# Kernel optimization log

Measured on AMD Instinct MI355X. Metric: run time of the kernel, lower is better.

Reference implementation:

```python
import jax, jax.numpy as jnp
import numpy as np


def setup_inputs() -> dict:
    key = jax.random.key(0)
    k1, k2 = jax.random.split(key)
    inputs = jax.random.normal(k1, (4, 128, 64, 64), dtype=jnp.float32)
    # binary hole mask (1 = known background, 0 = hole), broadcast over channels
    mask = jnp.round(jax.random.uniform(k2, (4, 1, 64, 64), dtype=jnp.float32))
    return {"inputs": inputs, "mask": mask}


def reference(inputs, mask):
    # SFFA contextual attention with 1x1 dynamic kernels.
    # Note: in the original torch code the 1x1 conv with padding=1 produces
    # border scores that conv_transpose2d with padding=1 crops away exactly,
    # so the math reduces to per-pixel matmul + softmax + matmul.
    bz, nc, h, w = inputs.shape
    N = h * w
    background = inputs * mask                              # [b, c, h, w]
    # dynamic kernels: one nc-dim vector per background pixel (patch)
    K = background.reshape(bz, nc, N).transpose(0, 2, 1) + 1e-7   # [b, N, c]
    Kn = K / jnp.sqrt(jnp.sum(K * K, axis=2, keepdims=True))      # l2-normalized
    feat = inputs.reshape(bz, nc, N)                        # [b, c, N]
    scores = jnp.einsum('bpc,bcn->bpn', Kn, feat)           # [b, N(patch), N(pixel)]
    attn = jax.nn.softmax(scores, axis=1)                   # softmax over patches p
    agg = jnp.einsum('bpc,bpn->bcn', K, attn).reshape(bz, nc, h, w)
    return background + agg * (1.0 - mask)
```

## Files before the change

### kernel.cpp

```cpp
#include <hip/hip_runtime.h>
#include <hip/hip_bf16.h>

typedef __attribute__((ext_vector_type(8))) short bf16x8;
typedef __attribute__((ext_vector_type(4))) float f32x4;

#define NPIX 4096
#define NC   128
#define RS128 0.08838834764831845f

#define GL2LDS(g, l) __builtin_amdgcn_global_load_lds( \
    (const __attribute__((address_space(1))) void*)(g), \
    (__attribute__((address_space(3))) void*)(l), 16, 0, 0)

__global__ __launch_bounds__(1024) void sffa_prep(
    const float* __restrict__ x, const float* __restrict__ mask,
    ushort* __restrict__ KnW, ushort* __restrict__ QW, ushort* __restrict__ VtW,
    float* __restrict__ s0c, int* __restrict__ pixQ, int* __restrict__ cnts,
    float* __restrict__ out)
{
    __shared__ float xs[128][69];
    __shared__ float ms[64];
    __shared__ float rinv[64];
    __shared__ float ssum[64];
    __shared__ float2 part[16][64];
    __shared__ int se[64];
    __shared__ int bgn[64];
    __shared__ int tinfo[2];
    __shared__ int wredP[16], wredT[16];
    const int tid = threadIdx.x;
    const int b = blockIdx.x >> 6, nblk = blockIdx.x & 63;
    const int n0 = nblk * 64;
    const float* xb = x + (size_t)b * NC * NPIX;
    float* ob = out + (size_t)b * NC * NPIX;

    #pragma unroll
    for (int it = 0; it < 2; ++it) {
        int e4 = it * 1024 + tid;
        int c = e4 >> 4, n4 = (e4 & 15) * 4;
        float4 v = *(const float4*)(xb + (size_t)c * NPIX + n0 + n4);
        xs[c][n4+0] = v.x; xs[c][n4+1] = v.y; xs[c][n4+2] = v.z; xs[c][n4+3] = v.w;
        *(float4*)(ob + (size_t)c * NPIX + n0 + n4) = v;
    }
    if (tid < 16) {
        float4 mv = *(const float4*)(mask + (size_t)b * NPIX + n0 + tid * 4);
        ms[tid*4+0] = mv.x; ms[tid*4+1] = mv.y; ms[tid*4+2] = mv.z; ms[tid*4+3] = mv.w;
    }
    {
        const int lane = tid & 63, w = tid >> 6;
        float4 mv = *(const float4*)(mask + (size_t)b * NPIX + tid * 4);
        int f0 = mv.x < 0.5f ? 0x10000 : 1;
        int f1 = mv.y < 0.5f ? 0x10000 : 1;
        int f2 = mv.z < 0.5f ? 0x10000 : 1;
        int f3 = mv.w < 0.5f ? 0x10000 : 1;
        int p0 = tid * 4;
        int pre = 0, tot = f0 + f1 + f2 + f3;
        if (p0 + 0 < n0) pre += f0;
        if (p0 + 1 < n0) pre += f1;
        if (p0 + 2 < n0) pre += f2;
        if (p0 + 3 < n0) pre += f3;
        #pragma unroll
        for (int d = 1; d < 64; d <<= 1) {
            pre += __shfl_xor(pre, d);
            tot += __shfl_xor(tot, d);
        }
        if (lane == 0) { wredP[w] = pre; wredT[w] = tot; }
    }
    __syncthreads();
    if (tid < 64) {
        int vP = (tid < 16) ? wredP[tid] : 0;
        int vT = (tid < 16) ? wredT[tid] : 0;
        #pragma unroll
        for (int d = 1; d < 16; d <<= 1) {
            vP += __shfl_xor(vP, d);
            vT += __shfl_xor(vT, d);
        }
        int base  = __shfl(vP, 0);
        int total = __shfl(vT, 0);
        if (tid == 0 && nblk == 0) {
            cnts[b * 2]     = total & 0xffff;
            cnts[b * 2 + 1] = total >> 16;
        }
        int f = ms[tid] > 0.5f ? 1 : 0x10000;
        int s = f;
        #pragma unroll
        for (int d = 1; d < 64; d <<= 1) {
            int t = __shfl_up(s, d);
            if (tid >= d) s += t;
        }
        se[tid] = base + s - f;
    }
    __syncthreads();
    {
        int p = tid & 63, qd = tid >> 6;
        float m = ms[p];
        float s2 = 0.f, s1 = 0.f;
        #pragma unroll
        for (int i = 0; i < 8; ++i) {
            float xv = xs[qd*8 + i][p];
            float k = fmaf(xv, m, 1e-7f);
            s2 = fmaf(k, k, s2);
            s1 += xv;
        }
        part[qd][p] = make_float2(s2, s1);
    }
    __syncthreads();
    if (tid < 64) {
        float s2 = 0.f, s1 = 0.f;
        #pragma unroll
        for (int k = 0; k < 16; ++k) { float2 t = part[k][tid]; s2 += t.x; s1 += t.y; }
        rinv[tid] = rsqrtf(s2);
        ssum[tid] = s1 * RS128;
    }
    __syncthreads();
    #pragma unroll
    for (int it = 0; it < 4; ++it) {
        int e2 = it * 1024 + tid;
        int n = e2 >> 6, cp = (e2 & 63) * 2;
        int pe = se[n];
        float x0 = xs[cp][n], x1 = xs[cp+1][n];
        if (ms[n] > 0.5f) {
            int slot = pe & 0xffff;
            float k0 = x0 + 1e-7f, k1 = x1 + 1e-7f;
            float r = rinv[n];
            __hip_bfloat162 kn;
            kn.x = __float2bfloat16(k0 * r); kn.y = __float2bfloat16(k1 * r);
            *(__hip_bfloat162*)(KnW + ((size_t)b * NPIX + slot) * NC + cp) = kn;
        } else {
            int slot = pe >> 16;
            __hip_bfloat162 q;
            q.x = __float2bfloat16(x0); q.y = __float2bfloat16(x1);
            *(__hip_bfloat162*)(QW + ((size_t)b * NPIX + slot) * NC + cp) = q;
        }
    }
    if (tid < 64) {
        if (ms[tid] < 0.5f) {
            int slot = se[tid] >> 16;
            s0c [(size_t)b * NPIX + slot] = ssum[tid];
            pixQ[(size_t)b * NPIX + slot] = n0 + tid;
        } else {
            bgn[(se[tid] & 0xffff) - (se[0] & 0xffff)] = tid;
        }
    }
    if (tid == 0) {
        tinfo[0] = se[0] & 0xffff;
        tinfo[1] = (se[63] & 0xffff) + (ms[63] > 0.5f ? 1 : 0) - (se[0] & 0xffff);
    }
    __syncthreads();
    {
        const int s0b = tinfo[0], nbg = tinfo[1];
        const int j = tid & 63, cg = tid >> 6;
        if (j < nbg) {
            int n = bgn[j];
            ushort* vcol = VtW + (size_t)b * NC * NPIX + s0b + j;
            #pragma unroll
            for (int cc = 0; cc < 8; ++cc) {
                int c = cg * 8 + cc;
                __hip_bfloat16 h = __float2bfloat16(xs[c][n] + 1e-7f);
                vcol[(size_t)c * NPIX] = *(ushort*)&h;
            }
        }
    }
}

#define L_BUF 32768
#define L_P   65536
#define L_ML  75776
#define L_SZ  76800

__global__ __launch_bounds__(512, 4) void sffa_attn(
    const ushort* __restrict__ KnW, const ushort* __restrict__ QW,
    const ushort* __restrict__ VtW, const int* __restrict__ cnts,
    ushort* __restrict__ partW, float* __restrict__ mlW, int KS)
{
    __shared__ __align__(16) char smem[L_SZ];
    const int tid  = threadIdx.x;
    const int w = tid >> 6, lane = tid & 63;
    const int l15 = lane & 15, g = lane >> 4;
    const int bx = (int)blockIdx.x;
    const int per = 64 * KS;
    const int b = bx / per;
    const int rem = bx - b * per;
    const int qblk = rem / KS, ks = rem - (rem / KS) * KS;
    const int q0 = qblk * 64;
    const int cntK = cnts[b * 2], cntQ = cnts[b * 2 + 1];
    if (q0 >= cntQ) return;
    const int blk = (b * 64 + qblk) * KS + ks;

    const int nk64 = (cntK + 63) >> 6;
    const int tpk  = (nk64 + KS - 1) / KS;
    const int t0   = ks * tpk;
    const int NTK  = min(t0 + tpk, nk64) - t0;

    if (NTK <= 0) {
        unsigned* pz = (unsigned*)(partW + (size_t)blk * 8192);
        #pragma unroll
        for (int i = 0; i < 8; ++i) pz[i * 512 + tid] = 0u;
        if (tid < 64)
            *(float2*)(mlW + ((size_t)blk * 64 + tid) * 2) = make_float2(-1e30f, 0.f);
        return;
    }

    const int half = w >> 2;
    const int wq   = w & 3;
    const int kbase = t0 * 64;

    const ushort* Knb = KnW + (size_t)b * NPIX * NC;
    const ushort* Vtb = VtW + (size_t)b * NC * NPIX;

    bf16x8 qf[4];
    {
        const ushort* Qrow = QW + ((size_t)b * NPIX + q0 + wq * 16 + l15) * NC;
        #pragma unroll
        for (int kc = 0; kc < 4; ++kc)
            qf[kc] = *(const bf16x8*)(Qrow + 32 * kc + 8 * g);
    }

    const int rK = tid >> 4;
    const char* srcK = (const char*)(Knb + (size_t)(kbase + rK) * NC)
                     + (((tid & 15) ^ (rK & 15)) << 4);
    const int rV = tid >> 3;
    const char* srcV = (const char*)(Vtb + (size_t)rV * NPIX + kbase)
                     + (((tid & 7) ^ (rV & 7)) << 4);
    char* d0 = smem + tid * 16;

    GL2LDS(srcK,        d0);
    GL2LDS(srcK + 8192, d0 + 8192);
    GL2LDS(srcV,                           d0 + 16384);
    GL2LDS(srcV + (size_t)64 * NPIX * 2,   d0 + 24576);
    __syncthreads();

    f32x4 acc[8];
    const f32x4 fzero = {0.f, 0.f, 0.f, 0.f};
    #pragma unroll
    for (int i = 0; i < 8; ++i) acc[i] = fzero;
    float mrun = -1e30f, lrun = 0.f;
    char* Pw = smem + L_P + w * 1280;

    for (int kt = 0; kt < NTK; ++kt) {
        if (kt + 1 < NTK) {
            char* nb = smem + ((kt + 1) & 1) * L_BUF + tid * 16;
            const char* sK = srcK + (size_t)(kt + 1) * 16384;
            const char* sV = srcV + (size_t)(kt + 1) * 128;
            GL2LDS(sK,        nb);
            GL2LDS(sK + 8192, nb + 8192);
            GL2LDS(sV,                         nb + 16384);
            GL2LDS(sV + (size_t)64 * NPIX * 2, nb + 24576);
        }
        char* bb = smem + (kt & 1) * L_BUF;
        f32x4 sa0 = fzero, sa1 = fzero;
        {
            const char* rb0 = bb + (half * 32 + l15) * 256;
            const char* rb1 = rb0 + 4096;
            const int sw = l15 << 4;
            __builtin_amdgcn_s_setprio(1);
            #pragma unroll
            for (int kc = 0; kc < 4; ++kc) {
                int off = (64 * kc + 16 * g) ^ sw;
                bf16x8 a0 = *(const bf16x8*)(rb0 + off);
                bf16x8 a1 = *(const bf16x8*)(rb1 + off);
                sa0 = __builtin_amdgcn_mfma_f32_16x16x32_bf16(a0, qf[kc], sa0, 0, 0, 0);
                sa1 = __builtin_amdgcn_mfma_f32_16x16x32_bf16(a1, qf[kc], sa1, 0, 0, 0);
            }
            __builtin_amdgcn_s_setprio(0);
        }
        {
            int kg0 = (t0 + kt) * 64;
            if (kg0 + 64 > cntK) {
                int kb = cntK - kg0;
                int kr = half * 32 + 4 * g;
                #pragma unroll
                for (int r = 0; r < 4; ++r) {
                    if (kr + r >= kb)      sa0[r] = -3e38f;
                    if (kr + 16 + r >= kb) sa1[r] = -3e38f;
                }
            }
        }
        float tmax = fmaxf(fmaxf(fmaxf(sa0[0], sa0[1]), fmaxf(sa0[2], sa0[3])),
                           fmaxf(fmaxf(sa1[0], sa1[1]), fmaxf(sa1[2], sa1[3])));
        tmax = fmaxf(tmax, __shfl_xor(tmax, 16));
        tmax = fmaxf(tmax, __shfl_xor(tmax, 32));
        bool grow = !__all(tmax <= mrun + 8.f);
        float mnew = grow ? fmaxf(mrun, tmax) : mrun;
        float p0[4], p1[4];
        float ts = 0.f;
        #pragma unroll
        for (int r = 0; r < 4; ++r) { p0[r] = __expf(sa0[r] - mnew); ts += p0[r]; }
        #pragma unroll
        for (int r = 0; r < 4; ++r) { p1[r] = __expf(sa1[r] - mnew); ts += p1[r]; }
        ts += __shfl_xor(ts, 16);
        ts += __shfl_xor(ts, 32);
        if (grow) {
            float sc = __expf(mrun - mnew);
            lrun = lrun * sc + ts;
            float scr[4];
            #pragma unroll
            for (int r = 0; r < 4; ++r) scr[r] = __shfl(sc, 4 * g + r);
            #pragma unroll
            for (int ct = 0; ct < 8; ++ct) {
                acc[ct][0] *= scr[0]; acc[ct][1] *= scr[1];
                acc[ct][2] *= scr[2]; acc[ct][3] *= scr[3];
            }
            mrun = mnew;
        } else {
            lrun += ts;
        }
        union { __hip_bfloat162 h; unsigned u; } ua0, ua1, ub0, ub1;
        ua0.h.x = __float2bfloat16(p0[0]); ua0.h.y = __float2bfloat16(p0[1]);
        ua1.h.x = __float2bfloat16(p0[2]); ua1.h.y = __float2bfloat16(p0[3]);
        ub0.h.x = __float2bfloat16(p1[0]); ub0.h.y = __float2bfloat16(p1[1]);
        ub1.h.x = __float2bfloat16(p1[2]); ub1.h.y = __float2bfloat16(p1[3]);
        *(int2*)(Pw + l15 * 80 +      8 * g) = make_int2((int)ua0.u, (int)ua1.u);
        *(int2*)(Pw + l15 * 80 + 32 + 8 * g) = make_int2((int)ub0.u, (int)ub1.u);
        bf16x8 pf = *(const bf16x8*)(Pw + l15 * 80 + 16 * g);
        {
            const char* vb = bb + 16384;
            __builtin_amdgcn_s_setprio(1);
            #pragma unroll
            for (int ct = 0; ct < 8; ++ct) {
                int c = 16 * ct + l15;
                bf16x8 vf = *(const bf16x8*)(vb + c * 128 +
                                             ((64 * half + 16 * g) ^ ((c & 7) << 4)));
                acc[ct] = __builtin_amdgcn_mfma_f32_16x16x32_bf16(pf, vf, acc[ct], 0, 0, 0);
            }
            __builtin_amdgcn_s_setprio(0);
        }
        __syncthreads();
    }

    float* ma = (float*)(smem + L_ML);
    float* la = ma + 64; float* mb = la + 64; float* lb = mb + 64;
    const int q = wq * 16 + l15;
    if (g == 0) {
        if (half == 0) { ma[q] = mrun; la[q] = lrun; }
        else           { mb[q] = mrun; lb[q] = lrun; }
    }
    __syncthreads();
    float* agg = (float*)smem;
    {
        float mstar = fmaxf(ma[q], mb[q]);
        float f = __expf(mrun - mstar);
        float fr[4];
        #pragma unroll
        for (int r = 0; r < 4; ++r) fr[r] = __shfl(f, 4 * g + r);
        if (half == 1) {
            #pragma unroll
            for (int ct = 0; ct < 8; ++ct) {
                int c = 16 * ct + l15;
                #pragma unroll
                for (int r = 0; r < 4; ++r)
                    agg[c * 68 + wq * 16 + 4 * g + r] = acc[ct][r] * fr[r];
            }
        }
        __syncthreads();
        if (half == 0) {
            #pragma unroll
            for (int ct = 0; ct < 8; ++ct) {
                int c = 16 * ct + l15;
                #pragma unroll
                for (int r = 0; r < 4; ++r) {
                    int idx = c * 68 + wq * 16 + 4 * g + r;
                    agg[idx] = acc[ct][r] * fr[r] + agg[idx];
                }
            }
        }
    }
    __syncthreads();
    if (tid < 64) {
        float M = fmaxf(ma[tid], mb[tid]);
        float ls = la[tid] * __expf(ma[tid] - M) + lb[tid] * __expf(mb[tid] - M);
        *(float2*)(mlW + ((size_t)blk * 64 + tid) * 2) = make_float2(M, ls);
    }
    ushort* pdst = partW + (size_t)blk * 8192;
    #pragma unroll
    for (int it = 0; it < 8; ++it) {
        int idx = it * 512 + tid;
        int c = idx >> 5, n2 = (idx & 31) * 2;
        __hip_bfloat162 h;
        h.x = __float2bfloat16(agg[c * 68 + n2]);
        h.y = __float2bfloat16(agg[c * 68 + n2 + 1]);
        *(__hip_bfloat162*)(pdst + c * 64 + n2) = h;
    }
}

__global__ __launch_bounds__(256) void sffa_comb(
    const ushort* __restrict__ partW, const float* __restrict__ mlW,
    const float* __restrict__ s0c, const int* __restrict__ pixQ,
    const int* __restrict__ cnts, float* __restrict__ out, int KS)
{
    __shared__ float wgtL[4][64];
    __shared__ int pixnL[64];
    const int tid = threadIdx.x;
    const int bx = blockIdx.x;
    const int b = bx >> 7, qb = (bx >> 1) & 63, ch = bx & 1;
    const int cntK = cnts[b * 2], cntQ = cnts[b * 2 + 1];
    if (qb * 64 >= cntQ) return;
    const int blkbase = (b * 64 + qb) * KS;
    const float m0f = (float)(NPIX - cntK);

    if (tid < 64) {
        int slot = qb * 64 + tid;
        int pix = -1;
        if (slot < cntQ) {
            pix = pixQ[(size_t)b * NPIX + slot];
            float s0 = s0c[(size_t)b * NPIX + slot];
            float M = s0;
            float2 mls[4];
            #pragma unroll
            for (int k = 0; k < 4; ++k) {
                if (k < KS) {
                    mls[k] = *(const float2*)(mlW + ((size_t)(blkbase + k) * 64 + tid) * 2);
                    M = fmaxf(M, mls[k].x);
                }
            }
            float L = m0f * __expf(s0 - M);
            #pragma unroll
            for (int k = 0; k < 4; ++k)
                if (k < KS) L += mls[k].y * __expf(mls[k].x - M);
            float Li = 1.f / L;
            #pragma unroll
            for (int k = 0; k < 4; ++k)
                if (k < KS) wgtL[k][tid] = __expf(mls[k].x - M) * Li;
        }
        pixnL[tid] = pix;
    }
    __syncthreads();

    float* ob = out + ((size_t)b * NC + ch * 64) * NPIX;
    const ushort* pb = partW + (size_t)blkbase * 8192 + ch * 4096;
    #pragma unroll
    for (int it = 0; it < 2; ++it) {
        int idx = it * 256 + tid;
        int c = idx >> 3, grp = idx & 7;
        float v[8] = {0.f,0.f,0.f,0.f,0.f,0.f,0.f,0.f};
        #pragma unroll
        for (int k = 0; k < 4; ++k) {
            if (k < KS) {
                ushort u[8];
                *(int4*)u = *(const int4*)(pb + (size_t)k * 8192 + c * 64 + grp * 8);
                #pragma unroll
                for (int j = 0; j < 8; ++j)
                    v[j] = fmaf(__uint_as_float((unsigned)u[j] << 16),
                                wgtL[k][grp * 8 + j], v[j]);
            }
        }
        #pragma unroll
        for (int j = 0; j < 8; ++j) {
            int pix = pixnL[grp * 8 + j];
            if (pix >= 0) ob[(size_t)c * NPIX + pix] = v[j];
        }
    }
}

extern "C" void kernel_launch(void* const* d_in, const int* in_sizes, int n_in,
                              void* d_out, int out_size, void* d_ws, size_t ws_size,
                              hipStream_t stream) {
    const float* x    = (const float*)d_in[0];
    const float* mask = (const float*)d_in[1];
    char* ws = (char*)d_ws;
    const size_t MBy = 1024 * 1024;
    const size_t KBy = 1024;

    ushort* KnW = (ushort*)(ws);
    ushort* QW  = (ushort*)(ws + 4 * MBy);
    ushort* VtW = (ushort*)(ws + 8 * MBy);

    size_t need4 = 12 * MBy + 16 * MBy + 1 * MBy;
    int KS = (ws_size >= need4) ? 4 : 2;
    ushort* partW = (ushort*)(ws + 12 * MBy);
    char* tail = ws + 12 * MBy + (size_t)KS * 4 * MBy;
    float* mlW  = (float*)(tail);
    float* s0c  = (float*)(tail + 576 * KBy);
    int*   pixQ = (int*)(tail + 640 * KBy);
    int*   cnts = (int*)(tail + 704 * KBy);

    sffa_prep <<<256, 1024, 0, stream>>>(x, mask, KnW, QW, VtW, s0c, pixQ, cnts,
                                         (float*)d_out);
    sffa_attn <<<4 * 64 * KS, 512, 0, stream>>>(KnW, QW, VtW, cnts, partW, mlW, KS);
    sffa_comb <<<4 * 128, 256, 0, stream>>>(partW, mlW, s0c, pixQ, cnts,
                                            (float*)d_out, KS);
}
```

Baseline: 54.56 us.

## Single-buffer attention LDS and raise key split to six for occupancy

The attention kernel drops its double-buffered K/V LDS staging in favour of one buffer that is refilled after each tile's compute under a barrier. This shrinks shared memory per block from about 75KB to about 43KB, so the launch bound can rise to 6 blocks per CU. The key split is fixed at 6 instead of a runtime 2 or 4, giving more parallel blocks, with the combine kernel and workspace layout adjusted to match. In exchange, global-to-LDS loads no longer overlap compute within a block, and the workspace-size fallback is removed, which assumes the larger partial buffer always fits.

Result: slower. 64.39 us (+18.0%).

```diff
diff --git a/kernel.cpp b/kernel.cpp
--- a/kernel.cpp
+++ b/kernel.cpp
@@ -7,6 +7,7 @@
 #define NPIX 4096
 #define NC   128
 #define RS128 0.08838834764831845f
+#define KSP  6
 
 #define GL2LDS(g, l) __builtin_amdgcn_global_load_lds( \
     (const __attribute__((address_space(1))) void*)(g), \
@@ -162,32 +163,32 @@
     }
 }
 
-#define L_BUF 32768
-#define L_P   65536
-#define L_ML  75776
-#define L_SZ  76800
-
-__global__ __launch_bounds__(512, 4) void sffa_attn(
+#define L_V   16384
+#define L_P   32768
+#define L_ML  43008
+#define L_SZ  44032
+
+__global__ __launch_bounds__(512, 6) void sffa_attn(
     const ushort* __restrict__ KnW, const ushort* __restrict__ QW,
     const ushort* __restrict__ VtW, const int* __restrict__ cnts,
-    ushort* __restrict__ partW, float* __restrict__ mlW, int KS)
+    ushort* __restrict__ partW, float* __restrict__ mlW)
 {
     __shared__ __align__(16) char smem[L_SZ];
     const int tid  = threadIdx.x;
     const int w = tid >> 6, lane = tid & 63;
     const int l15 = lane & 15, g = lane >> 4;
     const int bx = (int)blockIdx.x;
-    const int per = 64 * KS;
+    const int per = 64 * KSP;
     const int b = bx / per;
     const int rem = bx - b * per;
-    const int qblk = rem / KS, ks = rem - (rem / KS) * KS;
+    const int qblk = rem / KSP, ks = rem - (rem / KSP) * KSP;
     const int q0 = qblk * 64;
     const int cntK = cnts[b * 2], cntQ = cnts[b * 2 + 1];
     if (q0 >= cntQ) return;
-    const int blk = (b * 64 + qblk) * KS + ks;
+    const int blk = (b * 64 + qblk) * KSP + ks;
 
     const int nk64 = (cntK + 63) >> 6;
-    const int tpk  = (nk64 + KS - 1) / KS;
+    const int tpk  = (nk64 + KSP - 1) / KSP;
     const int t0   = ks * tpk;
     const int NTK  = min(t0 + tpk, nk64) - t0;
 
@@ -237,19 +238,9 @@
     char* Pw = smem + L_P + w * 1280;
 
     for (int kt = 0; kt < NTK; ++kt) {
-        if (kt + 1 < NTK) {
-            char* nb = smem + ((kt + 1) & 1) * L_BUF + tid * 16;
-            const char* sK = srcK + (size_t)(kt + 1) * 16384;
-            const char* sV = srcV + (size_t)(kt + 1) * 128;
-            GL2LDS(sK,        nb);
-            GL2LDS(sK + 8192, nb + 8192);
-            GL2LDS(sV,                         nb + 16384);
-            GL2LDS(sV + (size_t)64 * NPIX * 2, nb + 24576);
-        }
-        char* bb = smem + (kt & 1) * L_BUF;
         f32x4 sa0 = fzero, sa1 = fzero;
         {
-            const char* rb0 = bb + (half * 32 + l15) * 256;
+            const char* rb0 = smem + (half * 32 + l15) * 256;
             const char* rb1 = rb0 + 4096;
             const int sw = l15 << 4;
             __builtin_amdgcn_s_setprio(1);
@@ -313,7 +304,7 @@
         *(int2*)(Pw + l15 * 80 + 32 + 8 * g) = make_int2((int)ub0.u, (int)ub1.u);
         bf16x8 pf = *(const bf16x8*)(Pw + l15 * 80 + 16 * g);
         {
-            const char* vb = bb + 16384;
+            const char* vb = smem + L_V;
             __builtin_amdgcn_s_setprio(1);
             #pragma unroll
             for (int ct = 0; ct < 8; ++ct) {
@@ -325,6 +316,15 @@
             __builtin_amdgcn_s_setprio(0);
         }
         __syncthreads();
+        if (kt + 1 < NTK) {
+            const char* sK = srcK + (size_t)(kt + 1) * 16384;
+            const char* sV = srcV + (size_t)(kt + 1) * 128;
+            GL2LDS(sK,        d0);
+            GL2LDS(sK + 8192, d0 + 8192);
+            GL2LDS(sV,                         d0 + 16384);
+            GL2LDS(sV + (size_t)64 * NPIX * 2, d0 + 24576);
+            __syncthreads();
+        }
     }
 
     float* ma = (float*)(smem + L_ML);
@@ -385,16 +385,16 @@
 __global__ __launch_bounds__(256) void sffa_comb(
     const ushort* __restrict__ partW, const float* __restrict__ mlW,
     const float* __restrict__ s0c, const int* __restrict__ pixQ,
-    const int* __restrict__ cnts, float* __restrict__ out, int KS)
+    const int* __restrict__ cnts, float* __restrict__ out)
 {
-    __shared__ float wgtL[4][64];
+    __shared__ float wgtL[KSP][64];
     __shared__ int pixnL[64];
     const int tid = threadIdx.x;
     const int bx = blockIdx.x;
     const int b = bx >> 7, qb = (bx >> 1) & 63, ch = bx & 1;
     const int cntK = cnts[b * 2], cntQ = cnts[b * 2 + 1];
     if (qb * 64 >= cntQ) return;
-    const int blkbase = (b * 64 + qb) * KS;
+    const int blkbase = (b * 64 + qb) * KSP;
     const float m0f = (float)(NPIX - cntK);
 
     if (tid < 64) {
@@ -404,22 +404,19 @@
             pix = pixQ[(size_t)b * NPIX + slot];
             float s0 = s0c[(size_t)b * NPIX + slot];
             float M = s0;
-            float2 mls[4];
-            #pragma unroll
-            for (int k = 0; k < 4; ++k) {
-                if (k < KS) {
-                    mls[k] = *(const float2*)(mlW + ((size_t)(blkbase + k) * 64 + tid) * 2);
-                    M = fmaxf(M, mls[k].x);
-                }
+            float2 mls[KSP];
+            #pragma unroll
+            for (int k = 0; k < KSP; ++k) {
+                mls[k] = *(const float2*)(mlW + ((size_t)(blkbase + k) * 64 + tid) * 2);
+                M = fmaxf(M, mls[k].x);
             }
             float L = m0f * __expf(s0 - M);
             #pragma unroll
-            for (int k = 0; k < 4; ++k)
-                if (k < KS) L += mls[k].y * __expf(mls[k].x - M);
+            for (int k = 0; k < KSP; ++k) L += mls[k].y * __expf(mls[k].x - M);
             float Li = 1.f / L;
             #pragma unroll
-            for (int k = 0; k < 4; ++k)
-                if (k < KS) wgtL[k][tid] = __expf(mls[k].x - M) * Li;
+            for (int k = 0; k < KSP; ++k)
+                wgtL[k][tid] = __expf(mls[k].x - M) * Li;
         }
         pixnL[tid] = pix;
     }
@@ -433,15 +430,13 @@
         int c = idx >> 3, grp = idx & 7;
         float v[8] = {0.f,0.f,0.f,0.f,0.f,0.f,0.f,0.f};
         #pragma unroll
-        for (int k = 0; k < 4; ++k) {
-            if (k < KS) {
-                ushort u[8];
-                *(int4*)u = *(const int4*)(pb + (size_t)k * 8192 + c * 64 + grp * 8);
-                #pragma unroll
-                for (int j = 0; j < 8; ++j)
-                    v[j] = fmaf(__uint_as_float((unsigned)u[j] << 16),
-                                wgtL[k][grp * 8 + j], v[j]);
-            }
+        for (int k = 0; k < KSP; ++k) {
+            ushort u[8];
+            *(int4*)u = *(const int4*)(pb + (size_t)k * 8192 + c * 64 + grp * 8);
+            #pragma unroll
+            for (int j = 0; j < 8; ++j)
+                v[j] = fmaf(__uint_as_float((unsigned)u[j] << 16),
+                            wgtL[k][grp * 8 + j], v[j]);
         }
         #pragma unroll
         for (int j = 0; j < 8; ++j) {
@@ -464,18 +459,16 @@
     ushort* QW  = (ushort*)(ws + 4 * MBy);
     ushort* VtW = (ushort*)(ws + 8 * MBy);
 
-    size_t need4 = 12 * MBy + 16 * MBy + 1 * MBy;
-    int KS = (ws_size >= need4) ? 4 : 2;
     ushort* partW = (ushort*)(ws + 12 * MBy);
-    char* tail = ws + 12 * MBy + (size_t)KS * 4 * MBy;
+    char* tail = ws + 12 * MBy + (size_t)(4 * 64 * KSP) * 16 * KBy;
     float* mlW  = (float*)(tail);
-    float* s0c  = (float*)(tail + 576 * KBy);
-    int*   pixQ = (int*)(tail + 640 * KBy);
-    int*   cnts = (int*)(tail + 704 * KBy);
+    float* s0c  = (float*)(tail + 1024 * KBy);
+    int*   pixQ = (int*)(tail + 1088 * KBy);
+    int*   cnts = (int*)(tail + 1152 * KBy);
 
     sffa_prep <<<256, 1024, 0, stream>>>(x, mask, KnW, QW, VtW, s0c, pixQ, cnts,
                                          (float*)d_out);
-    sffa_attn <<<4 * 64 * KS, 512, 0, stream>>>(KnW, QW, VtW, cnts, partW, mlW, KS);
+    sffa_attn <<<4 * 64 * KSP, 512, 0, stream>>>(KnW, QW, VtW, cnts, partW, mlW);
     sffa_comb <<<4 * 128, 256, 0, stream>>>(partW, mlW, s0c, pixQ, cnts,
-                                            (float*)d_out, KS);
+                                            (float*)d_out);
 }
```
